# Kernel tuning notes

Measured on AMD Instinct MI355X. Metric: run time of the kernel, lower is better.

The kernel has to match this reference:

```python
import jax, jax.numpy as jnp
import numpy as np

B, V, H, K = 2048, 4096, 1024, 5

def setup_inputs() -> dict:
    key = jax.random.key(0)
    k1, k2, k3, k4, k5, k6, k7 = jax.random.split(key, 7)
    return {
        "visible_example": (jax.random.uniform(k1, (B, V)) > 0.5).astype(jnp.float32),
        "b_v": jax.random.normal(k2, (V,), jnp.float32) * 0.1,
        "b_h": jax.random.normal(k3, (H,), jnp.float32) * 0.1,
        "W": jax.random.normal(k4, (V, H), jnp.float32) * 0.02,
        "u_h0": jax.random.uniform(k5, (B, H), jnp.float32),
        "u_v": jax.random.uniform(k6, (K // 2 + 1, B, V), jnp.float32),
        "u_h": jax.random.uniform(k7, (K // 2, B, H), jnp.float32),
    }

def reference(visible_example, b_v, b_h, W, u_h0, u_v, u_h):
    # score(v,h) = -energy = v.b_v + h.b_h + (v @ W) * h summed
    def score(v, h):
        return v @ b_v + h @ b_h + jnp.einsum('bv,vh,bh->b', v, W, h)  # [B]

    def bernoulli(p, u):
        # samples are detached in the original (requires_grad_(False))
        return jax.lax.stop_gradient((p > u).astype(jnp.float32))

    # positive phase: sample h | data
    h = bernoulli(jax.nn.sigmoid(b_h + visible_example @ W), u_h0)  # [B,H]
    log_prob_positive = score(visible_example, h)

    # K-step alternating Gibbs chain: v, h, v, h, v  (statically unrolled)
    v = visible_example
    vi = hi = 0
    for k in range(K):
        if k % 2 == 0:
            v = bernoulli(jax.nn.sigmoid(b_v + h @ W.T), u_v[vi]); vi += 1
        else:
            h = bernoulli(jax.nn.sigmoid(b_h + v @ W), u_h[hi]); hi += 1

    log_prob_negative = score(v, h)
    return log_prob_positive - log_prob_negative  # [B]
```

## Files before the change

### kernel.cpp

```cpp
#include <hip/hip_runtime.h>
#include <math.h>

#define B_DIM 2048
#define V_DIM 4096
#define H_DIM 1024

#define BM 128
#define BN 128
#define BK 16
#define KC 384
#define NPANEL_H 11
#define NPANEL_V 3

enum { ACC_NONE = 0, ACC_PREACT = 1, ACC_BIAS = 2 };

#define GLD_LDS16(gsrc, ldst)                                                  \
    __builtin_amdgcn_global_load_lds(                                          \
        (const __attribute__((address_space(1))) void*)(gsrc),                 \
        (__attribute__((address_space(3))) void*)(ldst), 16, 0, 0)

__global__ __launch_bounds__(256) void gemm_h_panel(
    const float* __restrict__ A,
    const float* __restrict__ W,
    float* __restrict__ P0,
    float* __restrict__ Prest)
{
    __shared__ float Bs[3][BK][BN];

    const int bn  = blockIdx.x * BN;
    const int bm  = blockIdx.y * BM;
    const int pan = blockIdx.z;
    const int k0  = pan * KC;
    const int klen = (V_DIM - k0 < KC) ? (V_DIM - k0) : KC;
    const int T = klen / BK;

    const int t  = threadIdx.x;
    const int tx = t & 15;
    const int ty = t >> 4;
    const int wav  = t >> 6;
    const int lane = t & 63;
    const int radd = lane >> 5;
    const int cadd = (lane & 31) * 4;

    const float* Wsrc = W + (size_t)(k0 + wav * 4 + radd) * H_DIM + bn + cadd;

    const float* A0 = A + (size_t)(bm + ty * 4) * V_DIM + k0;
    const float* A1 = A0 + (size_t)64 * V_DIM;

    float part[8][8];
#pragma unroll
    for (int i = 0; i < 8; i++)
#pragma unroll
        for (int j = 0; j < 8; j++) part[i][j] = 0.0f;

    GLD_LDS16(Wsrc,              &Bs[0][wav * 4 + 0][0]);
    GLD_LDS16(Wsrc + 2 * H_DIM,  &Bs[0][wav * 4 + 2][0]);

    int cur = 0, nxt = 1;
    for (int it = 0; it < T; ++it) {
        if (it + 1 < T) {
            const float* Ws = Wsrc + (size_t)(it + 1) * BK * H_DIM;
            GLD_LDS16(Ws,             &Bs[nxt][wav * 4 + 0][0]);
            GLD_LDS16(Ws + 2 * H_DIM, &Bs[nxt][wav * 4 + 2][0]);
            asm volatile("s_waitcnt vmcnt(2)" ::: "memory");
        } else {
            asm volatile("s_waitcnt vmcnt(0)" ::: "memory");
        }
        __builtin_amdgcn_s_barrier();
        __builtin_amdgcn_sched_barrier(0);
        const int kb = it * BK;
#pragma unroll
        for (int q = 0; q < 4; ++q) {
            float ak[4][8];
#pragma unroll
            for (int i = 0; i < 4; i++) {
                float4 v0 = *(const float4*)(A0 + (size_t)i * V_DIM + kb + q * 4);
                float4 v1 = *(const float4*)(A1 + (size_t)i * V_DIM + kb + q * 4);
                ak[0][i] = v0.x; ak[1][i] = v0.y; ak[2][i] = v0.z; ak[3][i] = v0.w;
                ak[0][i + 4] = v1.x; ak[1][i + 4] = v1.y; ak[2][i + 4] = v1.z; ak[3][i + 4] = v1.w;
            }
#pragma unroll
            for (int s = 0; s < 4; ++s) {
                const int k = q * 4 + s;
                float4 ya = *(const float4*)(&Bs[cur][k][tx * 4]);
                float4 yb = *(const float4*)(&Bs[cur][k][64 + tx * 4]);
                float bb[8] = {ya.x, ya.y, ya.z, ya.w, yb.x, yb.y, yb.z, yb.w};
#pragma unroll
                for (int i = 0; i < 8; i++)
#pragma unroll
                    for (int j = 0; j < 8; j++)
                        part[i][j] = fmaf(ak[s][i], bb[j], part[i][j]);
            }
        }
        cur = nxt;
        nxt = (nxt == 2) ? 0 : nxt + 1;
    }

    float* Pout = (pan == 0) ? P0 : (Prest + (size_t)(pan - 1) * B_DIM * H_DIM);
#pragma unroll
    for (int i = 0; i < 8; i++) {
        const int row = bm + ((i < 4) ? (ty * 4 + i) : (64 + ty * 4 + (i - 4)));
        float4 lo, hi;
        lo.x = part[i][0]; lo.y = part[i][1]; lo.z = part[i][2]; lo.w = part[i][3];
        hi.x = part[i][4]; hi.y = part[i][5]; hi.z = part[i][6]; hi.w = part[i][7];
        *(float4*)(&Pout[(size_t)row * H_DIM + bn + tx * 4])      = lo;
        *(float4*)(&Pout[(size_t)row * H_DIM + bn + 64 + tx * 4]) = hi;
    }
}

__global__ __launch_bounds__(256) void transpose_kernel(
    const float* __restrict__ in,
    float* __restrict__ outT)
{
    __shared__ float tile[64][65];
    const int c0 = blockIdx.x * 64;
    const int b0 = blockIdx.y * 64;
    const int tx = threadIdx.x & 15;
    const int ty = threadIdx.x >> 4;
#pragma unroll
    for (int rr = 0; rr < 4; ++rr) {
        const int row = ty + rr * 16;
        float4 v = *(const float4*)(in + (size_t)(b0 + row) * H_DIM + c0 + tx * 4);
        tile[row][tx * 4 + 0] = v.x;
        tile[row][tx * 4 + 1] = v.y;
        tile[row][tx * 4 + 2] = v.z;
        tile[row][tx * 4 + 3] = v.w;
    }
    __syncthreads();
#pragma unroll
    for (int rr = 0; rr < 4; ++rr) {
        const int row = ty + rr * 16;
        float4 v;
        v.x = tile[tx * 4 + 0][row];
        v.y = tile[tx * 4 + 1][row];
        v.z = tile[tx * 4 + 2][row];
        v.w = tile[tx * 4 + 3][row];
        *(float4*)(outT + (size_t)(c0 + row) * B_DIM + b0 + tx * 4) = v;
    }
}

__global__ __launch_bounds__(256) void gemm_vT_panel(
    const float* __restrict__ Wm,
    const float* __restrict__ hT,
    float* __restrict__ P0,
    float* __restrict__ Prest)
{
    __shared__ float Bs[3][BK][BN];

    const int bi  = blockIdx.x * BM;
    const int bb0 = blockIdx.y * BN;
    const int pan = blockIdx.z;
    const int k0  = pan * KC;
    const int klen = (H_DIM - k0 < KC) ? (H_DIM - k0) : KC;
    const int T = klen / BK;

    const int t  = threadIdx.x;
    const int tx = t & 15;
    const int ty = t >> 4;
    const int wav  = t >> 6;
    const int lane = t & 63;
    const int radd = lane >> 5;
    const int cadd = (lane & 31) * 4;

    const float* Hsrc = hT + (size_t)(k0 + wav * 4 + radd) * B_DIM + bb0 + cadd;

    const float* W0 = Wm + (size_t)(bi + ty * 4) * H_DIM + k0;
    const float* W1 = W0 + (size_t)64 * H_DIM;

    float part[8][8];
#pragma unroll
    for (int i = 0; i < 8; i++)
#pragma unroll
        for (int j = 0; j < 8; j++) part[i][j] = 0.0f;

    GLD_LDS16(Hsrc,              &Bs[0][wav * 4 + 0][0]);
    GLD_LDS16(Hsrc + 2 * B_DIM,  &Bs[0][wav * 4 + 2][0]);

    int cur = 0, nxt = 1;
    for (int it = 0; it < T; ++it) {
        if (it + 1 < T) {
            const float* Hs = Hsrc + (size_t)(it + 1) * BK * B_DIM;
            GLD_LDS16(Hs,             &Bs[nxt][wav * 4 + 0][0]);
            GLD_LDS16(Hs + 2 * B_DIM, &Bs[nxt][wav * 4 + 2][0]);
            asm volatile("s_waitcnt vmcnt(2)" ::: "memory");
        } else {
            asm volatile("s_waitcnt vmcnt(0)" ::: "memory");
        }
        __builtin_amdgcn_s_barrier();
        __builtin_amdgcn_sched_barrier(0);
        const int kb = it * BK;
#pragma unroll
        for (int q = 0; q < 4; ++q) {
            float ak[4][8];
#pragma unroll
            for (int i = 0; i < 4; i++) {
                float4 v0 = *(const float4*)(W0 + (size_t)i * H_DIM + kb + q * 4);
                float4 v1 = *(const float4*)(W1 + (size_t)i * H_DIM + kb + q * 4);
                ak[0][i] = v0.x; ak[1][i] = v0.y; ak[2][i] = v0.z; ak[3][i] = v0.w;
                ak[0][i + 4] = v1.x; ak[1][i + 4] = v1.y; ak[2][i + 4] = v1.z; ak[3][i + 4] = v1.w;
            }
#pragma unroll
            for (int s = 0; s < 4; ++s) {
                const int k = q * 4 + s;
                float4 ya = *(const float4*)(&Bs[cur][k][tx * 4]);
                float4 yb = *(const float4*)(&Bs[cur][k][64 + tx * 4]);
                float bb[8] = {ya.x, ya.y, ya.z, ya.w, yb.x, yb.y, yb.z, yb.w};
#pragma unroll
                for (int i = 0; i < 8; i++)
#pragma unroll
                    for (int j = 0; j < 8; j++)
                        part[i][j] = fmaf(ak[s][i], bb[j], part[i][j]);
            }
        }
        cur = nxt;
        nxt = (nxt == 2) ? 0 : nxt + 1;
    }

    float* Pout = (pan == 0) ? P0 : (Prest + (size_t)(pan - 1) * B_DIM * V_DIM);
#pragma unroll
    for (int j = 0; j < 8; j++) {
        const int bcol = bb0 + ((j < 4) ? (tx * 4 + j) : (64 + tx * 4 + (j - 4)));
        float4 lo, hi;
        lo.x = part[0][j]; lo.y = part[1][j]; lo.z = part[2][j]; lo.w = part[3][j];
        hi.x = part[4][j]; hi.y = part[5][j]; hi.z = part[6][j]; hi.w = part[7][j];
        *(float4*)(&Pout[(size_t)bcol * V_DIM + bi + ty * 4])      = lo;
        *(float4*)(&Pout[(size_t)bcol * V_DIM + bi + 64 + ty * 4]) = hi;
    }
}

__global__ __launch_bounds__(256) void combine_h(
    const float* P0,
    const float* __restrict__ Prest,
    const float* __restrict__ bh,
    const float* __restrict__ U,
    float* Hout,
    double* __restrict__ acc,
    const int mode)
{
    const int b = blockIdx.x;
    const int c = threadIdx.x * 4;
    const size_t BH  = (size_t)B_DIM * H_DIM;
    const size_t off = (size_t)b * H_DIM + c;

    float4 tot = *(const float4*)(P0 + off);
#pragma unroll
    for (int p = 1; p < NPANEL_H; p++) {
        float4 q = *(const float4*)(Prest + (size_t)(p - 1) * BH + off);
        tot.x += q.x; tot.y += q.y; tot.z += q.z; tot.w += q.w;
    }
    float4 bias = *(const float4*)(bh + c);
    float4 u    = *(const float4*)(U + off);

    float pre[4] = {bias.x + tot.x, bias.y + tot.y, bias.z + tot.z, bias.w + tot.w};
    float bb[4]  = {bias.x, bias.y, bias.z, bias.w};
    float uu[4]  = {u.x, u.y, u.z, u.w};
    float hv[4];
#pragma unroll
    for (int j = 0; j < 4; j++) {
        float pp = 1.0f / (1.0f + expf(-pre[j]));
        hv[j] = (pp > uu[j]) ? 1.0f : 0.0f;
    }
    float4 hout; hout.x = hv[0]; hout.y = hv[1]; hout.z = hv[2]; hout.w = hv[3];
    *(float4*)(Hout + off) = hout;

    if (mode != ACC_NONE) {
        double s = 0.0;
#pragma unroll
        for (int j = 0; j < 4; j++) {
            if (mode == ACC_PREACT) s += (double)hv[j] * (double)pre[j];
            else                    s += (double)hv[j] * (double)bb[j];
        }
#pragma unroll
        for (int offl = 32; offl >= 1; offl >>= 1) s += __shfl_xor(s, offl, 64);
        __shared__ double red[4];
        if ((threadIdx.x & 63) == 0) red[threadIdx.x >> 6] = s;
        __syncthreads();
        if (threadIdx.x == 0) acc[b] = red[0] + red[1] + red[2] + red[3];
    }
}

__global__ __launch_bounds__(256) void combine_v(
    const float* P0,
    const float* __restrict__ Prest,
    const float* __restrict__ bv,
    const float* __restrict__ U,
    float* Vout,
    double* __restrict__ acc,
    const int mode)
{
    const int b = blockIdx.x;
    const size_t BV = (size_t)B_DIM * V_DIM;
    double s = 0.0;

#pragma unroll
    for (int ch = 0; ch < 4; ++ch) {
        const int c = ch * 1024 + threadIdx.x * 4;
        const size_t off = (size_t)b * V_DIM + c;
        float4 tot = *(const float4*)(P0 + off);
        float4 q1  = *(const float4*)(Prest + off);
        float4 q2  = *(const float4*)(Prest + BV + off);
        tot.x += q1.x; tot.y += q1.y; tot.z += q1.z; tot.w += q1.w;
        tot.x += q2.x; tot.y += q2.y; tot.z += q2.z; tot.w += q2.w;

        float4 bias = *(const float4*)(bv + c);
        float4 u4   = *(const float4*)(U + off);
        float pre[4] = {bias.x + tot.x, bias.y + tot.y, bias.z + tot.z, bias.w + tot.w};
        float uu[4]  = {u4.x, u4.y, u4.z, u4.w};
        float vs[4];
#pragma unroll
        for (int j = 0; j < 4; j++) {
            float pp = 1.0f / (1.0f + expf(-pre[j]));
            vs[j] = (pp > uu[j]) ? 1.0f : 0.0f;
            if (mode == ACC_PREACT) s += (double)vs[j] * (double)pre[j];
        }
        float4 vst; vst.x = vs[0]; vst.y = vs[1]; vst.z = vs[2]; vst.w = vs[3];
        *(float4*)(Vout + off) = vst;
    }

    if (mode != ACC_NONE) {
#pragma unroll
        for (int offl = 32; offl >= 1; offl >>= 1) s += __shfl_xor(s, offl, 64);
        __shared__ double red[4];
        if ((threadIdx.x & 63) == 0) red[threadIdx.x >> 6] = s;
        __syncthreads();
        if (threadIdx.x == 0) acc[b] = red[0] + red[1] + red[2] + red[3];
    }
}

__global__ __launch_bounds__(256) void rowdot_kernel(
    const float* __restrict__ X, const float* __restrict__ w,
    double* __restrict__ out, const int N)
{
    const int b = blockIdx.x;
    const float* row = X + (size_t)b * N;
    double s = 0.0;
    for (int i = threadIdx.x; i < N / 4; i += blockDim.x) {
        float4 x = ((const float4*)row)[i];
        float4 ww = ((const float4*)w)[i];
        s = fma((double)x.x, (double)ww.x, s);
        s = fma((double)x.y, (double)ww.y, s);
        s = fma((double)x.z, (double)ww.z, s);
        s = fma((double)x.w, (double)ww.w, s);
    }
#pragma unroll
    for (int off = 32; off >= 1; off >>= 1) s += __shfl_xor(s, off, 64);
    __shared__ double red[4];
    if ((threadIdx.x & 63) == 0) red[threadIdx.x >> 6] = s;
    __syncthreads();
    if (threadIdx.x == 0) out[b] = red[0] + red[1] + red[2] + red[3];
}

__global__ void finalize_kernel(const double* __restrict__ vb,
                                const double* __restrict__ accpos,
                                const double* __restrict__ acchb,
                                const double* __restrict__ accneg,
                                float* __restrict__ out)
{
    int b = blockIdx.x * blockDim.x + threadIdx.x;
    if (b < B_DIM) out[b] = (float)(vb[b] + accpos[b] - acchb[b] - accneg[b]);
}

extern "C" void kernel_launch(void* const* d_in, const int* in_sizes, int n_in,
                              void* d_out, int out_size, void* d_ws, size_t ws_size,
                              hipStream_t stream) {
    (void)in_sizes; (void)n_in; (void)out_size; (void)ws_size;
    const float* visible = (const float*)d_in[0];
    const float* b_v     = (const float*)d_in[1];
    const float* b_h     = (const float*)d_in[2];
    const float* W       = (const float*)d_in[3];
    const float* u_h0    = (const float*)d_in[4];
    const float* u_v     = (const float*)d_in[5];
    const float* u_h     = (const float*)d_in[6];
    float* out = (float*)d_out;

    float* v_buf   = (float*)d_ws;
    float* h_buf   = v_buf + (size_t)B_DIM * V_DIM;
    double* acc_pos = (double*)(h_buf + (size_t)B_DIM * H_DIM);
    double* acc_hb  = acc_pos + B_DIM;
    double* acc_neg = acc_hb + B_DIM;
    double* vb      = acc_neg + B_DIM;
    float* Pextra   = (float*)(vb + B_DIM);
    float* hT       = Pextra + (size_t)10 * B_DIM * H_DIM;

    dim3 blk(256);
    dim3 gh(H_DIM / BN, B_DIM / BM, NPANEL_H);
    dim3 gv(V_DIM / BM, B_DIM / BN, NPANEL_V);
    dim3 gt(H_DIM / 64, B_DIM / 64);
    dim3 gc(B_DIM);

    rowdot_kernel<<<B_DIM, blk, 0, stream>>>(visible, b_v, vb, V_DIM);

    const size_t UV = (size_t)B_DIM * V_DIM;
    const size_t UH = (size_t)B_DIM * H_DIM;

    gemm_h_panel<<<gh, blk, 0, stream>>>(visible, W, h_buf, Pextra);
    combine_h<<<gc, blk, 0, stream>>>(h_buf, Pextra, b_h, u_h0, h_buf, acc_pos, ACC_PREACT);
    transpose_kernel<<<gt, blk, 0, stream>>>(h_buf, hT);
    gemm_vT_panel<<<gv, blk, 0, stream>>>(W, hT, v_buf, Pextra);
    combine_v<<<gc, blk, 0, stream>>>(v_buf, Pextra, b_v, u_v + 0 * UV, v_buf, nullptr, ACC_NONE);
    gemm_h_panel<<<gh, blk, 0, stream>>>(v_buf, W, h_buf, Pextra);
    combine_h<<<gc, blk, 0, stream>>>(h_buf, Pextra, b_h, u_h + 0 * UH, h_buf, nullptr, ACC_NONE);
    transpose_kernel<<<gt, blk, 0, stream>>>(h_buf, hT);
    gemm_vT_panel<<<gv, blk, 0, stream>>>(W, hT, v_buf, Pextra);
    combine_v<<<gc, blk, 0, stream>>>(v_buf, Pextra, b_v, u_v + 1 * UV, v_buf, nullptr, ACC_NONE);
    gemm_h_panel<<<gh, blk, 0, stream>>>(v_buf, W, h_buf, Pextra);
    combine_h<<<gc, blk, 0, stream>>>(h_buf, Pextra, b_h, u_h + 1 * UH, h_buf, acc_hb, ACC_BIAS);
    transpose_kernel<<<gt, blk, 0, stream>>>(h_buf, hT);
    gemm_vT_panel<<<gv, blk, 0, stream>>>(W, hT, v_buf, Pextra);
    combine_v<<<gc, blk, 0, stream>>>(v_buf, Pextra, b_v, u_v + 2 * UV, v_buf, acc_neg, ACC_PREACT);

    finalize_kernel<<<(B_DIM + 255) / 256, blk, 0, stream>>>(vb, acc_pos, acc_hb, acc_neg, out);
}
```

Measured before the change: 1.615 ms.

## Drop LDS staging in GEMMs and fuse h transpose into combine_h

Both panel GEMM kernels stop staging the shared B operand through a triple-buffered LDS pipeline with async global-to-LDS loads and barriers. Each thread now reads W or hT rows straight from global memory, relying on the cache for reuse across threads. The separate transpose kernel is removed, and combine_h writes the transposed h directly using strided scalar stores. This cuts barriers and one kernel launch, but risks more global and cache traffic in the GEMMs and uncoalesced writes of hT.

New measurement: 2.633 ms. 63.0% more time.

```diff
diff --git a/kernel.cpp b/kernel.cpp
--- a/kernel.cpp
+++ b/kernel.cpp
@@ -7,17 +7,11 @@
 
 #define BM 128
 #define BN 128
-#define BK 16
 #define KC 384
 #define NPANEL_H 11
 #define NPANEL_V 3
 
 enum { ACC_NONE = 0, ACC_PREACT = 1, ACC_BIAS = 2 };
-
-#define GLD_LDS16(gsrc, ldst)                                                  \
-    __builtin_amdgcn_global_load_lds(                                          \
-        (const __attribute__((address_space(1))) void*)(gsrc),                 \
-        (__attribute__((address_space(3))) void*)(ldst), 16, 0, 0)
 
 __global__ __launch_bounds__(256) void gemm_h_panel(
     const float* __restrict__ A,
@@ -25,27 +19,19 @@
     float* __restrict__ P0,
     float* __restrict__ Prest)
 {
-    __shared__ float Bs[3][BK][BN];
-
     const int bn  = blockIdx.x * BN;
     const int bm  = blockIdx.y * BM;
     const int pan = blockIdx.z;
     const int k0  = pan * KC;
     const int klen = (V_DIM - k0 < KC) ? (V_DIM - k0) : KC;
-    const int T = klen / BK;
 
     const int t  = threadIdx.x;
     const int tx = t & 15;
     const int ty = t >> 4;
-    const int wav  = t >> 6;
-    const int lane = t & 63;
-    const int radd = lane >> 5;
-    const int cadd = (lane & 31) * 4;
-
-    const float* Wsrc = W + (size_t)(k0 + wav * 4 + radd) * H_DIM + bn + cadd;
 
     const float* A0 = A + (size_t)(bm + ty * 4) * V_DIM + k0;
     const float* A1 = A0 + (size_t)64 * V_DIM;
+    const float* Wk = W + (size_t)k0 * H_DIM + bn;
 
     float part[8][8];
 #pragma unroll
@@ -53,37 +39,23 @@
 #pragma unroll
         for (int j = 0; j < 8; j++) part[i][j] = 0.0f;
 
-    GLD_LDS16(Wsrc,              &Bs[0][wav * 4 + 0][0]);
-    GLD_LDS16(Wsrc + 2 * H_DIM,  &Bs[0][wav * 4 + 2][0]);
-
-    int cur = 0, nxt = 1;
-    for (int it = 0; it < T; ++it) {
-        if (it + 1 < T) {
-            const float* Ws = Wsrc + (size_t)(it + 1) * BK * H_DIM;
-            GLD_LDS16(Ws,             &Bs[nxt][wav * 4 + 0][0]);
-            GLD_LDS16(Ws + 2 * H_DIM, &Bs[nxt][wav * 4 + 2][0]);
-            asm volatile("s_waitcnt vmcnt(2)" ::: "memory");
-        } else {
-            asm volatile("s_waitcnt vmcnt(0)" ::: "memory");
-        }
-        __builtin_amdgcn_s_barrier();
-        __builtin_amdgcn_sched_barrier(0);
-        const int kb = it * BK;
+    for (int kt = 0; kt < klen; kt += 16) {
 #pragma unroll
         for (int q = 0; q < 4; ++q) {
+            const int kb = kt + q * 4;
             float ak[4][8];
 #pragma unroll
             for (int i = 0; i < 4; i++) {
-                float4 v0 = *(const float4*)(A0 + (size_t)i * V_DIM + kb + q * 4);
-                float4 v1 = *(const float4*)(A1 + (size_t)i * V_DIM + kb + q * 4);
+                float4 v0 = *(const float4*)(A0 + (size_t)i * V_DIM + kb);
+                float4 v1 = *(const float4*)(A1 + (size_t)i * V_DIM + kb);
                 ak[0][i] = v0.x; ak[1][i] = v0.y; ak[2][i] = v0.z; ak[3][i] = v0.w;
                 ak[0][i + 4] = v1.x; ak[1][i + 4] = v1.y; ak[2][i + 4] = v1.z; ak[3][i + 4] = v1.w;
             }
 #pragma unroll
             for (int s = 0; s < 4; ++s) {
-                const int k = q * 4 + s;
-                float4 ya = *(const float4*)(&Bs[cur][k][tx * 4]);
-                float4 yb = *(const float4*)(&Bs[cur][k][64 + tx * 4]);
+                const float* Wrow = Wk + (size_t)(kb + s) * H_DIM;
+                float4 ya = *(const float4*)(Wrow + tx * 4);
+                float4 yb = *(const float4*)(Wrow + 64 + tx * 4);
                 float bb[8] = {ya.x, ya.y, ya.z, ya.w, yb.x, yb.y, yb.z, yb.w};
 #pragma unroll
                 for (int i = 0; i < 8; i++)
@@ -92,8 +64,6 @@
                         part[i][j] = fmaf(ak[s][i], bb[j], part[i][j]);
             }
         }
-        cur = nxt;
-        nxt = (nxt == 2) ? 0 : nxt + 1;
     }
 
     float* Pout = (pan == 0) ? P0 : (Prest + (size_t)(pan - 1) * B_DIM * H_DIM);
@@ -108,64 +78,25 @@
     }
 }
 
-__global__ __launch_bounds__(256) void transpose_kernel(
-    const float* __restrict__ in,
-    float* __restrict__ outT)
-{
-    __shared__ float tile[64][65];
-    const int c0 = blockIdx.x * 64;
-    const int b0 = blockIdx.y * 64;
-    const int tx = threadIdx.x & 15;
-    const int ty = threadIdx.x >> 4;
-#pragma unroll
-    for (int rr = 0; rr < 4; ++rr) {
-        const int row = ty + rr * 16;
-        float4 v = *(const float4*)(in + (size_t)(b0 + row) * H_DIM + c0 + tx * 4);
-        tile[row][tx * 4 + 0] = v.x;
-        tile[row][tx * 4 + 1] = v.y;
-        tile[row][tx * 4 + 2] = v.z;
-        tile[row][tx * 4 + 3] = v.w;
-    }
-    __syncthreads();
-#pragma unroll
-    for (int rr = 0; rr < 4; ++rr) {
-        const int row = ty + rr * 16;
-        float4 v;
-        v.x = tile[tx * 4 + 0][row];
-        v.y = tile[tx * 4 + 1][row];
-        v.z = tile[tx * 4 + 2][row];
-        v.w = tile[tx * 4 + 3][row];
-        *(float4*)(outT + (size_t)(c0 + row) * B_DIM + b0 + tx * 4) = v;
-    }
-}
-
 __global__ __launch_bounds__(256) void gemm_vT_panel(
     const float* __restrict__ Wm,
     const float* __restrict__ hT,
     float* __restrict__ P0,
     float* __restrict__ Prest)
 {
-    __shared__ float Bs[3][BK][BN];
-
     const int bi  = blockIdx.x * BM;
     const int bb0 = blockIdx.y * BN;
     const int pan = blockIdx.z;
     const int k0  = pan * KC;
     const int klen = (H_DIM - k0 < KC) ? (H_DIM - k0) : KC;
-    const int T = klen / BK;
 
     const int t  = threadIdx.x;
     const int tx = t & 15;
     const int ty = t >> 4;
-    const int wav  = t >> 6;
-    const int lane = t & 63;
-    const int radd = lane >> 5;
-    const int cadd = (lane & 31) * 4;
-
-    const float* Hsrc = hT + (size_t)(k0 + wav * 4 + radd) * B_DIM + bb0 + cadd;
 
     const float* W0 = Wm + (size_t)(bi + ty * 4) * H_DIM + k0;
     const float* W1 = W0 + (size_t)64 * H_DIM;
+    const float* Hk = hT + (size_t)k0 * B_DIM + bb0;
 
     float part[8][8];
 #pragma unroll
@@ -173,37 +104,23 @@
 #pragma unroll
         for (int j = 0; j < 8; j++) part[i][j] = 0.0f;
 
-    GLD_LDS16(Hsrc,              &Bs[0][wav * 4 + 0][0]);
-    GLD_LDS16(Hsrc + 2 * B_DIM,  &Bs[0][wav * 4 + 2][0]);
-
-    int cur = 0, nxt = 1;
-    for (int it = 0; it < T; ++it) {
-        if (it + 1 < T) {
-            const float* Hs = Hsrc + (size_t)(it + 1) * BK * B_DIM;
-            GLD_LDS16(Hs,             &Bs[nxt][wav * 4 + 0][0]);
-            GLD_LDS16(Hs + 2 * B_DIM, &Bs[nxt][wav * 4 + 2][0]);
-            asm volatile("s_waitcnt vmcnt(2)" ::: "memory");
-        } else {
-            asm volatile("s_waitcnt vmcnt(0)" ::: "memory");
-        }
-        __builtin_amdgcn_s_barrier();
-        __builtin_amdgcn_sched_barrier(0);
-        const int kb = it * BK;
+    for (int kt = 0; kt < klen; kt += 16) {
 #pragma unroll
         for (int q = 0; q < 4; ++q) {
+            const int kb = kt + q * 4;
             float ak[4][8];
 #pragma unroll
             for (int i = 0; i < 4; i++) {
-                float4 v0 = *(const float4*)(W0 + (size_t)i * H_DIM + kb + q * 4);
-                float4 v1 = *(const float4*)(W1 + (size_t)i * H_DIM + kb + q * 4);
+                float4 v0 = *(const float4*)(W0 + (size_t)i * H_DIM + kb);
+                float4 v1 = *(const float4*)(W1 + (size_t)i * H_DIM + kb);
                 ak[0][i] = v0.x; ak[1][i] = v0.y; ak[2][i] = v0.z; ak[3][i] = v0.w;
                 ak[0][i + 4] = v1.x; ak[1][i + 4] = v1.y; ak[2][i + 4] = v1.z; ak[3][i + 4] = v1.w;
             }
 #pragma unroll
             for (int s = 0; s < 4; ++s) {
-                const int k = q * 4 + s;
-                float4 ya = *(const float4*)(&Bs[cur][k][tx * 4]);
-                float4 yb = *(const float4*)(&Bs[cur][k][64 + tx * 4]);
+                const float* Hrow = Hk + (size_t)(kb + s) * B_DIM;
+                float4 ya = *(const float4*)(Hrow + tx * 4);
+                float4 yb = *(const float4*)(Hrow + 64 + tx * 4);
                 float bb[8] = {ya.x, ya.y, ya.z, ya.w, yb.x, yb.y, yb.z, yb.w};
 #pragma unroll
                 for (int i = 0; i < 8; i++)
@@ -212,8 +129,6 @@
                         part[i][j] = fmaf(ak[s][i], bb[j], part[i][j]);
             }
         }
-        cur = nxt;
-        nxt = (nxt == 2) ? 0 : nxt + 1;
     }
 
     float* Pout = (pan == 0) ? P0 : (Prest + (size_t)(pan - 1) * B_DIM * V_DIM);
@@ -234,6 +149,7 @@
     const float* __restrict__ bh,
     const float* __restrict__ U,
     float* Hout,
+    float* __restrict__ hTout,
     double* __restrict__ acc,
     const int mode)
 {
@@ -262,6 +178,10 @@
     }
     float4 hout; hout.x = hv[0]; hout.y = hv[1]; hout.z = hv[2]; hout.w = hv[3];
     *(float4*)(Hout + off) = hout;
+
+#pragma unroll
+    for (int e = 0; e < 4; e++)
+        hTout[(size_t)(c + e) * B_DIM + b] = hv[e];
 
     if (mode != ACC_NONE) {
         double s = 0.0;
@@ -385,7 +305,6 @@
     dim3 blk(256);
     dim3 gh(H_DIM / BN, B_DIM / BM, NPANEL_H);
     dim3 gv(V_DIM / BM, B_DIM / BN, NPANEL_V);
-    dim3 gt(H_DIM / 64, B_DIM / 64);
     dim3 gc(B_DIM);
 
     rowdot_kernel<<<B_DIM, blk, 0, stream>>>(visible, b_v, vb, V_DIM);
@@ -394,18 +313,15 @@
     const size_t UH = (size_t)B_DIM * H_DIM;
 
     gemm_h_panel<<<gh, blk, 0, stream>>>(visible, W, h_buf, Pextra);
-    combine_h<<<gc, blk, 0, stream>>>(h_buf, Pextra, b_h, u_h0, h_buf, acc_pos, ACC_PREACT);
-    transpose_kernel<<<gt, blk, 0, stream>>>(h_buf, hT);
+    combine_h<<<gc, blk, 0, stream>>>(h_buf, Pextra, b_h, u_h0, h_buf, hT, acc_pos, ACC_PREACT);
     gemm_vT_panel<<<gv, blk, 0, stream>>>(W, hT, v_buf, Pextra);
     combine_v<<<gc, blk, 0, stream>>>(v_buf, Pextra, b_v, u_v + 0 * UV, v_buf, nullptr, ACC_NONE);
     gemm_h_panel<<<gh, blk, 0, stream>>>(v_buf, W, h_buf, Pextra);
-    combine_h<<<gc, blk, 0, stream>>>(h_buf, Pextra, b_h, u_h + 0 * UH, h_buf, nullptr, ACC_NONE);
-    transpose_kernel<<<gt, blk, 0, stream>>>(h_buf, hT);
+    combine_h<<<gc, blk, 0, stream>>>(h_buf, Pextra, b_h, u_h + 0 * UH, h_buf, hT, nullptr, ACC_NONE);
     gemm_vT_panel<<<gv, blk, 0, stream>>>(W, hT, v_buf, Pextra);
     combine_v<<<gc, blk, 0, stream>>>(v_buf, Pextra, b_v, u_v + 1 * UV, v_buf, nullptr, ACC_NONE);
     gemm_h_panel<<<gh, blk, 0, stream>>>(v_buf, W, h_buf, Pextra);
-    combine_h<<<gc, blk, 0, stream>>>(h_buf, Pextra, b_h, u_h + 1 * UH, h_buf, acc_hb, ACC_BIAS);
-    transpose_kernel<<<gt, blk, 0, stream>>>(h_buf, hT);
+    combine_h<<<gc, blk, 0, stream>>>(h_buf, Pextra, b_h, u_h + 1 * UH, h_buf, hT, acc_hb, ACC_BIAS);
     gemm_vT_panel<<<gv, blk, 0, stream>>>(W, hT, v_buf, Pextra);
     combine_v<<<gc, blk, 0, stream>>>(v_buf, Pextra, b_v, u_v + 2 * UV, v_buf, acc_neg, ACC_PREACT);
 
```
